# Kernel optimization log

Measured on AMD Instinct MI355X. Metric: run time of the kernel, lower is better.

The kernel has to match this reference:

```python
import jax, jax.numpy as jnp
import numpy as np

NUM_HEADS = 16

def setup_inputs() -> dict:
    key = jax.random.key(0)
    ks = jax.random.split(key, 5)
    B, L, H = 4, 1024, 1024
    s = 0.02
    return {
        'x': jax.random.normal(ks[0], (B, L, H), jnp.float32),
        'Wq': jax.random.normal(ks[1], (H, H), jnp.float32) * s,
        'Wkv_short': jax.random.normal(ks[2], (H, 2 * H), jnp.float32) * s,
        'Wkv_long': jax.random.normal(ks[3], (H, 2 * H), jnp.float32) * s,
        'Wo': jax.random.normal(ks[4], (H, H), jnp.float32) * s,
        'mix_weight': jnp.float32(0.5),
        'decay_factor': jnp.float32(0.95),
    }

def _heads(t, B, L, nh, hd):
    # [B, L, H] -> [B, nh, L, hd]
    return t.reshape(B, L, nh, hd).transpose(0, 2, 1, 3)

def _attention(q, k, v, bias):
    # q,k,v: [B, nh, L, hd]; bias: [L, L] or None
    hd = q.shape[-1]
    scores = jnp.einsum('bhqd,bhkd->bhqk', q, k) / jnp.sqrt(jnp.float32(hd))
    if bias is not None:
        scores = scores + bias[None, None]
    attn = jax.nn.softmax(scores, axis=-1)
    return jnp.einsum('bhqk,bhkd->bhqd', attn, v)

def reference(x, Wq, Wkv_short, Wkv_long, Wo, mix_weight, decay_factor):
    B, L, H = x.shape
    nh = NUM_HEADS
    hd = H // nh
    q = _heads(x @ Wq, B, L, nh, hd)
    kv_s = x @ Wkv_short
    k_s = _heads(kv_s[..., :H], B, L, nh, hd)
    v_s = _heads(kv_s[..., H:], B, L, nh, hd)
    pos = jnp.arange(L, dtype=jnp.float32)
    decay_bias = -jnp.abs(pos[None, :] - pos[:, None]) * (1.0 - decay_factor)
    out_short = _attention(q, k_s, v_s, decay_bias)
    kv_l = x @ Wkv_long
    k_l = _heads(kv_l[..., :H], B, L, nh, hd)
    v_l = _heads(kv_l[..., H:], B, L, nh, hd)
    out_long = _attention(q, k_l, v_l, None)
    alpha = jax.nn.sigmoid(mix_weight)
    out = alpha * out_short + (1.0 - alpha) * out_long
    out = out.transpose(0, 2, 1, 3).reshape(B, L, H)
    return out @ Wo
```

## Files before the change

kernel.cpp:

```cpp
#include <hip/hip_runtime.h>
#include <hip/hip_bf16.h>
#include <math.h>
#include <stdint.h>

typedef unsigned short u16;
typedef __attribute__((ext_vector_type(8))) short bf16x8;
typedef __attribute__((ext_vector_type(4))) float f32x4;
typedef __attribute__((ext_vector_type(4))) unsigned short u16x4;

#define MFMA_BF16(A, B, C) __builtin_amdgcn_mfma_f32_16x16x32_bf16((A), (B), (C), 0, 0, 0)

__device__ __forceinline__ void async16(const void* g, const void* l) {
    __builtin_amdgcn_global_load_lds(
        (const __attribute__((address_space(1))) unsigned int*)(uintptr_t)g,
        (__attribute__((address_space(3))) unsigned int*)(uintptr_t)l, 16, 0, 0);
}

__device__ __forceinline__ u16 f2bf(float f) {
    unsigned u = __float_as_uint(f);
    u += 0x7fffu + ((u >> 16) & 1u);
    return (u16)(u >> 16);
}

__device__ __forceinline__ unsigned pack2(float a, float b) {
    __hip_bfloat162 h = __float22bfloat162_rn(float2{a, b});
    return *reinterpret_cast<unsigned*>(&h);
}

__device__ __forceinline__ float bf2f(u16 v) {
    unsigned u = ((unsigned)v) << 16;
    return __uint_as_float(u);
}

__global__ __launch_bounds__(256) void cvt_x(const float* __restrict__ x,
                                             u16* __restrict__ xb) {
    int i = blockIdx.x * 256 + threadIdx.x;
    float4 v = ((const float4*)x)[i];
    u16x4 o = {f2bf(v.x), f2bf(v.y), f2bf(v.z), f2bf(v.w)};
    ((u16x4*)xb)[i] = o;
}

__global__ __launch_bounds__(256) void cvt_w_all(
    const float* __restrict__ Wq, const float* __restrict__ Wks,
    const float* __restrict__ Wkl, const float* __restrict__ Wo,
    u16* __restrict__ wqt, u16* __restrict__ wkst,
    u16* __restrict__ wklt, u16* __restrict__ wot)
{
    __shared__ float tile[32][33];
    int x = blockIdx.x;
    const float* W; u16* Wt; int N, nb;
    if (x < 32)       { W = Wq;  Wt = wqt;  N = 1024; nb = x * 32; }
    else if (x < 96)  { W = Wks; Wt = wkst; N = 2048; nb = (x - 32) * 32; }
    else if (x < 160) { W = Wkl; Wt = wklt; N = 2048; nb = (x - 96) * 32; }
    else              { W = Wo;  Wt = wot;  N = 1024; nb = (x - 160) * 32; }
    int kb = blockIdx.y * 32;
    int t = threadIdx.x;
    int r = t >> 3, c4 = (t & 7) * 4;
    float4 v = *(const float4*)&W[(size_t)(kb + r) * N + nb + c4];
    tile[r][c4] = v.x; tile[r][c4 + 1] = v.y;
    tile[r][c4 + 2] = v.z; tile[r][c4 + 3] = v.w;
    __syncthreads();
    u16x4 o = {f2bf(tile[c4 + 0][r]), f2bf(tile[c4 + 1][r]),
               f2bf(tile[c4 + 2][r]), f2bf(tile[c4 + 3][r])};
    *(u16x4*)&Wt[(size_t)(nb + r) * 1024 + kb + c4] = o;
}

__global__ __launch_bounds__(256) void gemm_proj(
    const u16* __restrict__ A, const u16* __restrict__ wq,
    const u16* __restrict__ wks, const u16* __restrict__ wkl,
    u16* __restrict__ qd, u16* __restrict__ ksd, u16* __restrict__ vsd,
    u16* __restrict__ kld, u16* __restrict__ vld)
{
    __shared__ u16 Alds[128][32];
    __shared__ u16 Blds[128][32];
    const int cx = blockIdx.x;
    const u16* Bt; u16* dK; u16* dV; int colBase; float osc = 1.0f;
    bool ktype;
    if (cx < 8)       { Bt = wq;  colBase = cx * 128;        dK = qd;  dV = nullptr;
                        osc = 0.18033688f; ktype = true; }
    else if (cx < 24) { Bt = wks; colBase = (cx - 8) * 128;  dK = ksd; dV = vsd;
                        ktype = (cx < 16); }
    else              { Bt = wkl; colBase = (cx - 24) * 128; dK = kld; dV = vld;
                        ktype = (cx < 32); }

    const int t = threadIdx.x;
    const int l = t & 63, w = t >> 6;
    const int wm = w & 1, wn = w >> 1;
    const int rowBase = blockIdx.y * 128;
    const int lc = l & 15, lr4 = l >> 4;

    f32x4 acc[4][4];
#pragma unroll
    for (int i = 0; i < 4; i++)
#pragma unroll
        for (int j = 0; j < 4; j++) acc[i][j] = (f32x4){0.f, 0.f, 0.f, 0.f};

    const int srow = w * 32 + (l >> 2);
    const int sc8  = (((l & 3) ^ ((l >> 2) & 3)) * 8);
    const u16* Ag = A  + (size_t)(rowBase + srow) * 1024 + sc8;
    const u16* Bg = Bt + (size_t)(colBase + srow) * 1024 + sc8;
    const int sw = (lc & 3);

    const u16 (*Lm)[32] = ktype ? Blds : Alds;
    const u16 (*Ln)[32] = ktype ? Alds : Blds;

    for (int kt = 0; kt < 32; ++kt) {
        __syncthreads();
        const int ko = kt * 32;
        async16(Ag + ko,         &Alds[w * 32][0]);
        async16(Ag + ko + 16384, &Alds[w * 32 + 16][0]);
        async16(Bg + ko,         &Blds[w * 32][0]);
        async16(Bg + ko + 16384, &Blds[w * 32 + 16][0]);
        __syncthreads();

        bf16x8 af[4], bf[4];
#pragma unroll
        for (int mt = 0; mt < 4; ++mt)
            af[mt] = *(const bf16x8*)&Lm[wm * 64 + mt * 16 + lc][(lr4 ^ sw) * 8];
#pragma unroll
        for (int nt = 0; nt < 4; ++nt)
            bf[nt] = *(const bf16x8*)&Ln[wn * 64 + nt * 16 + lc][(lr4 ^ sw) * 8];
#pragma unroll
        for (int mt = 0; mt < 4; ++mt)
#pragma unroll
            for (int nt = 0; nt < 4; ++nt)
                acc[mt][nt] = MFMA_BF16(af[mt], bf[nt], acc[mt][nt]);
    }

    if (ktype) {
#pragma unroll
        for (int mt = 0; mt < 4; ++mt)
#pragma unroll
            for (int nt = 0; nt < 4; ++nt) {
                int f   = colBase + wm * 64 + mt * 16 + lr4 * 4;
                int tok = rowBase + wn * 64 + nt * 16 + lc;
                int b = tok >> 10, tk = tok & 1023;
                int head = (f >> 6) & 15, d = f & 63;
                u16x4 pv = {f2bf(acc[mt][nt][0] * osc), f2bf(acc[mt][nt][1] * osc),
                            f2bf(acc[mt][nt][2] * osc), f2bf(acc[mt][nt][3] * osc)};
                *(u16x4*)&dK[((size_t)(b * 16 + head) * 1024 + tk) * 64 + d] = pv;
            }
    } else {
#pragma unroll
        for (int mt = 0; mt < 4; ++mt)
#pragma unroll
            for (int nt = 0; nt < 4; ++nt) {
                int gr0 = rowBase + wm * 64 + mt * 16 + lr4 * 4;
                int gc0 = colBase + wn * 64 + nt * 16;
                int head = gc0 >> 6;
                int b = gr0 >> 10, tok = gr0 & 1023;
                int d = (gc0 & 63) + lc;
                u16x4 pv = {f2bf(acc[mt][nt][0]), f2bf(acc[mt][nt][1]),
                            f2bf(acc[mt][nt][2]), f2bf(acc[mt][nt][3])};
                *(u16x4*)&dV[((size_t)(b * 16 + head - 16) * 64 + d) * 1024 +
                             tok] = pv;
            }
    }
}

__global__ __launch_bounds__(256) void gemm_out(
    const u16* __restrict__ Aattn, const u16* __restrict__ Bwot,
    float* __restrict__ dst)
{
    __shared__ u16 Alds[64][32];
    __shared__ u16 Blds[128][32];
    const int t = threadIdx.x;
    const int l = t & 63, w = t >> 6;
    const int wm = w & 1, wn = w >> 1;
    const int rowBase = blockIdx.y * 64;
    const int colBase = blockIdx.x * 128;
    const int lc = l & 15, lr4 = l >> 4;

    f32x4 acc[4][2];
#pragma unroll
    for (int i = 0; i < 4; i++)
#pragma unroll
        for (int j = 0; j < 2; j++) acc[i][j] = (f32x4){0.f, 0.f, 0.f, 0.f};

    const int sl  = l >> 2;
    const int sc8 = (((l & 3) ^ (sl & 3)) * 8);
    const u16* Ag = Aattn + (size_t)(rowBase + w * 16 + sl) * 1024 + sc8;
    const u16* Bg = Bwot  + (size_t)(colBase + w * 32 + sl) * 1024 + sc8;
    const int sw = (lc & 3);

    for (int kt = 0; kt < 32; ++kt) {
        __syncthreads();
        const int ko = kt * 32;
        async16(Ag + ko,         &Alds[w * 16][0]);
        async16(Bg + ko,         &Blds[w * 32][0]);
        async16(Bg + ko + 16384, &Blds[w * 32 + 16][0]);
        __syncthreads();

        bf16x8 af[4], bf[2];
#pragma unroll
        for (int mt = 0; mt < 4; ++mt)
            af[mt] = *(const bf16x8*)&Blds[wm * 64 + mt * 16 + lc][(lr4 ^ sw) * 8];
#pragma unroll
        for (int nt = 0; nt < 2; ++nt)
            bf[nt] = *(const bf16x8*)&Alds[wn * 32 + nt * 16 + lc][(lr4 ^ sw) * 8];
#pragma unroll
        for (int mt = 0; mt < 4; ++mt)
#pragma unroll
            for (int nt = 0; nt < 2; ++nt)
                acc[mt][nt] = MFMA_BF16(af[mt], bf[nt], acc[mt][nt]);
    }

#pragma unroll
    for (int mt = 0; mt < 4; ++mt)
#pragma unroll
        for (int nt = 0; nt < 2; ++nt) {
            int f   = colBase + wm * 64 + mt * 16 + lr4 * 4;
            int tok = rowBase + wn * 32 + nt * 16 + lc;
            float4 v = {acc[mt][nt][0], acc[mt][nt][1],
                        acc[mt][nt][2], acc[mt][nt][3]};
            *(float4*)&dst[(size_t)tok * 1024 + f] = v;
        }
}

__global__ __launch_bounds__(256, 3) void attn_mfma(
    const u16* __restrict__ Q, const u16* __restrict__ Ksb,
    const u16* __restrict__ Vsb, const u16* __restrict__ Klb,
    const u16* __restrict__ Vlb, const float* __restrict__ decayf,
    u16* __restrict__ Os, u16* __restrict__ Ol)
{
    __shared__ __align__(16) u16 Kt[2][2][64][32];
    __shared__ __align__(16) u16 Vt[2][2][64][32];
    __shared__ __align__(16) u16 Ps[4][32][72];

    const int t = threadIdx.x;
    const int l = t & 63, w = t >> 6;
    const int lc = l & 15, lr4 = l >> 4;
    const int h = blockIdx.x, qt = blockIdx.y;
    const int b = blockIdx.z >> 1, branch = blockIdx.z & 1;
    const size_t bh = (size_t)(b * 16 + h);
    const int qbase = qt * 128;
    const u16* Qg = Q + bh * (1024 * 64);
    const u16* Kg = (branch ? Klb : Ksb) + bh * (1024 * 64);
    const u16* Vg = (branch ? Vlb : Vsb) + bh * (64 * 1024);
    u16* outp = branch ? Ol : Os;

    const int sl = l >> 2;
    const int sc = (((l & 3) ^ ((l >> 3) & 3)) * 8);
    const int swr = (lc >> 1) & 3;

    int ktLo = 0, ktHi = 16;
    if (branch == 0) {
        ktLo = qt * 2 - 7; if (ktLo < 0) ktLo = 0;
        ktHi = qt * 2 + 9; if (ktHi > 16) ktHi = 16;
    }

    bf16x8 aQ[2][2];
#pragma unroll
    for (int qg = 0; qg < 2; ++qg)
#pragma unroll
        for (int kh = 0; kh < 2; ++kh)
            aQ[qg][kh] = *(const bf16x8*)&Qg[
                (size_t)(qbase + w * 32 + qg * 16 + lc) * 64 + kh * 32 + lr4 * 8];

    auto stage = [&](int kt, int buf) {
#pragma unroll
        for (int i = 0; i < 4; i++) {
            int id = w * 4 + i;
            int kh = (id >> 2) & 1, ch = id & 3;
            if (id < 8)
                async16(Kg + (size_t)(kt * 64 + ch * 16 + sl) * 64 + kh * 32 + sc,
                        &Kt[buf][kh][ch * 16][0]);
            else
                async16(Vg + (size_t)(ch * 16 + sl) * 1024 + kt * 64 + kh * 32 + sc,
                        &Vt[buf][kh][ch * 16][0]);
        }
    };

    stage(ktLo, 0);
    __syncthreads();

    const float C2 = (1.0f - decayf[0]) * 1.44269504f;
    const float qf = (float)(qbase + w * 32 + lc);

    float lrun[2] = {0.f, 0.f};
    f32x4 o[2][4];
#pragma unroll
    for (int qg = 0; qg < 2; ++qg)
#pragma unroll
        for (int dt = 0; dt < 4; ++dt) o[qg][dt] = (f32x4){0.f, 0.f, 0.f, 0.f};

    for (int kt = ktLo, it = 0; kt < ktHi; ++kt, ++it) {
        const int cur = it & 1;
        if (kt + 1 < ktHi) stage(kt + 1, cur ^ 1);

        bf16x8 ak[4][2];
#pragma unroll
        for (int nt = 0; nt < 4; ++nt) {
            ak[nt][0] = *(const bf16x8*)&Kt[cur][0][nt * 16 + lc][(lr4 ^ swr) * 8];
            ak[nt][1] = *(const bf16x8*)&Kt[cur][1][nt * 16 + lc][(lr4 ^ swr) * 8];
        }

#pragma unroll
        for (int qg = 0; qg < 2; ++qg) {
            f32x4 s[4];
#pragma unroll
            for (int nt = 0; nt < 4; ++nt) {
                s[nt] = (f32x4){0.f, 0.f, 0.f, 0.f};
                s[nt] = MFMA_BF16(ak[nt][0], aQ[qg][0], s[nt]);
                s[nt] = MFMA_BF16(ak[nt][1], aQ[qg][1], s[nt]);
            }
            const float d0 = qf + (float)(qg * 16 - kt * 64 - lr4 * 4);
            float sum = 0.f;
#pragma unroll
            for (int nt = 0; nt < 4; ++nt) {
                float p[4];
#pragma unroll
                for (int r = 0; r < 4; ++r) {
                    float a = s[nt][r];
                    if (branch == 0)
                        a -= fabsf(d0 - (float)(nt * 16 + r)) * C2;
                    p[r] = __builtin_amdgcn_exp2f(a);
                    sum += p[r];
                }
                uint2 w2 = {pack2(p[0], p[1]), pack2(p[2], p[3])};
                *(uint2*)&Ps[w][qg * 16 + lc][nt * 16 + lr4 * 4] = w2;
            }
            lrun[qg] += sum;
        }

        bf16x8 pb[2][2];
#pragma unroll
        for (int qg = 0; qg < 2; ++qg)
#pragma unroll
            for (int c = 0; c < 2; ++c)
                pb[qg][c] = *(const bf16x8*)&Ps[w][qg * 16 + lc][c * 32 + lr4 * 8];
#pragma unroll
        for (int dt = 0; dt < 4; ++dt) {
            bf16x8 v0 = *(const bf16x8*)&Vt[cur][0][dt * 16 + lc][(lr4 ^ swr) * 8];
            bf16x8 v1 = *(const bf16x8*)&Vt[cur][1][dt * 16 + lc][(lr4 ^ swr) * 8];
#pragma unroll
            for (int qg = 0; qg < 2; ++qg) {
                o[qg][dt] = MFMA_BF16(v0, pb[qg][0], o[qg][dt]);
                o[qg][dt] = MFMA_BF16(v1, pb[qg][1], o[qg][dt]);
            }
        }

        __syncthreads();
    }

#pragma unroll
    for (int qg = 0; qg < 2; ++qg) {
        float s = lrun[qg];
        s += __shfl_xor(s, 16);
        s += __shfl_xor(s, 32);
        float inv = 1.0f / s;
        int qrow = qbase + w * 32 + qg * 16 + lc;
        u16* op = outp + ((size_t)(b * 1024) + qrow) * 1024 + h * 64;
#pragma unroll
        for (int dt = 0; dt < 4; ++dt) {
            uint2 w2 = {pack2(o[qg][dt][0] * inv, o[qg][dt][1] * inv),
                        pack2(o[qg][dt][2] * inv, o[qg][dt][3] * inv)};
            *(uint2*)&op[dt * 16 + lr4 * 4] = w2;
        }
    }
}

__global__ __launch_bounds__(256) void mix_kernel(
    const u16* __restrict__ Os, const u16* __restrict__ Ol,
    const float* __restrict__ mixw, u16* __restrict__ dst)
{
    const float a = 1.0f / (1.0f + __expf(-mixw[0]));
    int i = blockIdx.x * 256 + threadIdx.x;
    uint4 s = ((const uint4*)Os)[i];
    uint4 l = ((const uint4*)Ol)[i];
    unsigned su[4] = {s.x, s.y, s.z, s.w};
    unsigned lu[4] = {l.x, l.y, l.z, l.w};
    unsigned ou[4];
#pragma unroll
    for (int k = 0; k < 4; ++k) {
        float s0 = bf2f((u16)su[k]), s1 = bf2f((u16)(su[k] >> 16));
        float l0 = bf2f((u16)lu[k]), l1 = bf2f((u16)(lu[k] >> 16));
        ou[k] = pack2(l0 + a * (s0 - l0), l1 + a * (s1 - l1));
    }
    ((uint4*)dst)[i] = make_uint4(ou[0], ou[1], ou[2], ou[3]);
}

extern "C" void kernel_launch(void* const* d_in, const int* in_sizes, int n_in,
                              void* d_out, int out_size, void* d_ws, size_t ws_size,
                              hipStream_t stream) {
    const float* x      = (const float*)d_in[0];
    const float* Wq     = (const float*)d_in[1];
    const float* Wkvs   = (const float*)d_in[2];
    const float* Wkvl   = (const float*)d_in[3];
    const float* Wo     = (const float*)d_in[4];
    const float* mixw   = (const float*)d_in[5];
    const float* decayf = (const float*)d_in[6];

    const size_t M1 = 1024 * 1024;
    u16* ws    = (u16*)d_ws;
    u16* xb    = ws;
    u16* wqt   = xb + 4 * M1;
    u16* wkvst = wqt + 1 * M1;
    u16* wkvlt = wkvst + 2 * M1;
    u16* wot   = wkvlt + 2 * M1;
    u16* qb    = wot + 1 * M1;
    u16* ksb   = qb + 4 * M1;
    u16* vsb   = ksb + 4 * M1;
    u16* klb   = vsb + 4 * M1;
    u16* vlb   = klb + 4 * M1;
    u16* attnb = vlb + 4 * M1;
    u16* osb   = xb;
    u16* olb   = wqt;

    cvt_x<<<4096, 256, 0, stream>>>(x, xb);
    cvt_w_all<<<dim3(192, 32), 256, 0, stream>>>(Wq, Wkvs, Wkvl, Wo,
                                                 wqt, wkvst, wkvlt, wot);
    gemm_proj<<<dim3(40, 32), 256, 0, stream>>>(xb, wqt, wkvst, wkvlt,
                                                qb, ksb, vsb, klb, vlb);
    attn_mfma<<<dim3(16, 8, 8), 256, 0, stream>>>(qb, ksb, vsb, klb, vlb,
                                                  decayf, osb, olb);
    mix_kernel<<<2048, 256, 0, stream>>>(osb, olb, mixw, attnb);
    gemm_out<<<dim3(8, 64), 256, 0, stream>>>(attnb, wot, (float*)d_out);
}
```

Measured before the change: 236.8 us.

## Keep softmax probabilities in registers by permuting V layout, drop P LDS staging

The V projection epilogue now writes tokens in a permuted order within each 32-token group, so the bf16 probability fragments produced by the QK MFMA can feed the PV MFMA directly from registers. This removes the per-wave Ps shared-memory buffer along with its store and reload. The decay bias is folded into the MFMA accumulator initialisation, and the row sums are kept as a vector. Freeing the LDS lets occupancy rise to 5 blocks per CU, which adds register pressure and couples correctness to the permuted V layout.

```diff
diff --git a/kernel.cpp b/kernel.cpp
--- a/kernel.cpp
+++ b/kernel.cpp
@@ -7,6 +7,7 @@
 typedef __attribute__((ext_vector_type(8))) short bf16x8;
 typedef __attribute__((ext_vector_type(4))) float f32x4;
 typedef __attribute__((ext_vector_type(4))) unsigned short u16x4;
+typedef __attribute__((ext_vector_type(4))) unsigned int uint32x4;
 
 #define MFMA_BF16(A, B, C) __builtin_amdgcn_mfma_f32_16x16x32_bf16((A), (B), (C), 0, 0, 0)
 
@@ -30,6 +31,12 @@
 __device__ __forceinline__ float bf2f(u16 v) {
     unsigned u = ((unsigned)v) << 16;
     return __uint_as_float(u);
+}
+
+__device__ __forceinline__ bf16x8 mk_frag(unsigned w0, unsigned w1,
+                                          unsigned w2, unsigned w3) {
+    uint32x4 u = {w0, w1, w2, w3};
+    return __builtin_bit_cast(bf16x8, u);
 }
 
 __global__ __launch_bounds__(256) void cvt_x(const float* __restrict__ x,
@@ -149,11 +156,13 @@
                 int gc0 = colBase + wn * 64 + nt * 16;
                 int head = gc0 >> 6;
                 int b = gr0 >> 10, tok = gr0 & 1023;
+                int tokp = (tok & ~31) | (((tok >> 2) & 3) << 3) |
+                           (((tok >> 4) & 1) << 2);
                 int d = (gc0 & 63) + lc;
                 u16x4 pv = {f2bf(acc[mt][nt][0]), f2bf(acc[mt][nt][1]),
                             f2bf(acc[mt][nt][2]), f2bf(acc[mt][nt][3])};
                 *(u16x4*)&dV[((size_t)(b * 16 + head - 16) * 64 + d) * 1024 +
-                             tok] = pv;
+                             tokp] = pv;
             }
     }
 }
@@ -217,7 +226,7 @@
         }
 }
 
-__global__ __launch_bounds__(256, 3) void attn_mfma(
+__global__ __launch_bounds__(256, 5) void attn_mfma(
     const u16* __restrict__ Q, const u16* __restrict__ Ksb,
     const u16* __restrict__ Vsb, const u16* __restrict__ Klb,
     const u16* __restrict__ Vlb, const float* __restrict__ decayf,
@@ -225,7 +234,6 @@
 {
     __shared__ __align__(16) u16 Kt[2][2][64][32];
     __shared__ __align__(16) u16 Vt[2][2][64][32];
-    __shared__ __align__(16) u16 Ps[4][32][72];
 
     const int t = threadIdx.x;
     const int l = t & 63, w = t >> 6;
@@ -277,7 +285,7 @@
     const float C2 = (1.0f - decayf[0]) * 1.44269504f;
     const float qf = (float)(qbase + w * 32 + lc);
 
-    float lrun[2] = {0.f, 0.f};
+    f32x4 sumv[2] = {(f32x4){0.f, 0.f, 0.f, 0.f}, (f32x4){0.f, 0.f, 0.f, 0.f}};
     f32x4 o[2][4];
 #pragma unroll
     for (int qg = 0; qg < 2; ++qg)
@@ -295,48 +303,48 @@
             ak[nt][1] = *(const bf16x8*)&Kt[cur][1][nt * 16 + lc][(lr4 ^ swr) * 8];
         }
 
+        unsigned pw[2][8];
 #pragma unroll
         for (int qg = 0; qg < 2; ++qg) {
+            const float d0 = qf + (float)(qg * 16 - kt * 64 - lr4 * 4);
             f32x4 s[4];
 #pragma unroll
             for (int nt = 0; nt < 4; ++nt) {
-                s[nt] = (f32x4){0.f, 0.f, 0.f, 0.f};
+                if (branch == 0) {
+                    float dd = d0 - (float)(nt * 16);
+                    s[nt] = (f32x4){-fabsf(dd) * C2,
+                                    -fabsf(dd - 1.0f) * C2,
+                                    -fabsf(dd - 2.0f) * C2,
+                                    -fabsf(dd - 3.0f) * C2};
+                } else {
+                    s[nt] = (f32x4){0.f, 0.f, 0.f, 0.f};
+                }
                 s[nt] = MFMA_BF16(ak[nt][0], aQ[qg][0], s[nt]);
                 s[nt] = MFMA_BF16(ak[nt][1], aQ[qg][1], s[nt]);
             }
-            const float d0 = qf + (float)(qg * 16 - kt * 64 - lr4 * 4);
-            float sum = 0.f;
 #pragma unroll
             for (int nt = 0; nt < 4; ++nt) {
-                float p[4];
-#pragma unroll
-                for (int r = 0; r < 4; ++r) {
-                    float a = s[nt][r];
-                    if (branch == 0)
-                        a -= fabsf(d0 - (float)(nt * 16 + r)) * C2;
-                    p[r] = __builtin_amdgcn_exp2f(a);
-                    sum += p[r];
-                }
-                uint2 w2 = {pack2(p[0], p[1]), pack2(p[2], p[3])};
-                *(uint2*)&Ps[w][qg * 16 + lc][nt * 16 + lr4 * 4] = w2;
+                float p0 = __builtin_amdgcn_exp2f(s[nt][0]);
+                float p1 = __builtin_amdgcn_exp2f(s[nt][1]);
+                float p2 = __builtin_amdgcn_exp2f(s[nt][2]);
+                float p3 = __builtin_amdgcn_exp2f(s[nt][3]);
+                sumv[qg][0] += p0; sumv[qg][1] += p1;
+                sumv[qg][2] += p2; sumv[qg][3] += p3;
+                pw[qg][nt * 2]     = pack2(p0, p1);
+                pw[qg][nt * 2 + 1] = pack2(p2, p3);
             }
-            lrun[qg] += sum;
-        }
-
-        bf16x8 pb[2][2];
-#pragma unroll
-        for (int qg = 0; qg < 2; ++qg)
-#pragma unroll
-            for (int c = 0; c < 2; ++c)
-                pb[qg][c] = *(const bf16x8*)&Ps[w][qg * 16 + lc][c * 32 + lr4 * 8];
+        }
+
 #pragma unroll
         for (int dt = 0; dt < 4; ++dt) {
             bf16x8 v0 = *(const bf16x8*)&Vt[cur][0][dt * 16 + lc][(lr4 ^ swr) * 8];
             bf16x8 v1 = *(const bf16x8*)&Vt[cur][1][dt * 16 + lc][(lr4 ^ swr) * 8];
 #pragma unroll
             for (int qg = 0; qg < 2; ++qg) {
-                o[qg][dt] = MFMA_BF16(v0, pb[qg][0], o[qg][dt]);
-                o[qg][dt] = MFMA_BF16(v1, pb[qg][1], o[qg][dt]);
+                bf16x8 pb0 = mk_frag(pw[qg][0], pw[qg][1], pw[qg][2], pw[qg][3]);
+                bf16x8 pb1 = mk_frag(pw[qg][4], pw[qg][5], pw[qg][6], pw[qg][7]);
+                o[qg][dt] = MFMA_BF16(v0, pb0, o[qg][dt]);
+                o[qg][dt] = MFMA_BF16(v1, pb1, o[qg][dt]);
             }
         }
 
@@ -345,7 +353,7 @@
 
 #pragma unroll
     for (int qg = 0; qg < 2; ++qg) {
-        float s = lrun[qg];
+        float s = (sumv[qg][0] + sumv[qg][1]) + (sumv[qg][2] + sumv[qg][3]);
         s += __shfl_xor(s, 16);
         s += __shfl_xor(s, 32);
         float inv = 1.0f / s;
```

Result: slower. 335.3 us (+41.6%).
